# Optimization experiments

Hardware: AMD Instinct MI355X
Metric: run time of the kernel (lower is better)

Reference implementation:

```python
import jax, jax.numpy as jnp
import numpy as np

EPS = 1e-6

def _phi(x):
    # ELU + 1 feature map: strictly positive
    return jax.nn.elu(x) + 1.0

def setup_inputs() -> dict:
    key = jax.random.key(0)
    kq, kk, kv = jax.random.split(key, 3)
    B, T, H, D = 4, 8192, 16, 64
    q = jax.random.normal(kq, (B, T, H, D), dtype=jnp.float32)
    k = jax.random.normal(kk, (B, T, H, D), dtype=jnp.float32)
    v = jax.random.normal(kv, (B, T, H, D), dtype=jnp.float32)
    return {"q": q, "k": k, "v": v}

def _linear_attention(q, k, v):
    # q,k,v: [B,T,H,D] -> out [B,T,H,D]
    phi_q = _phi(q)
    phi_k = _phi(k)
    # time-major for scan: [T,B,H,D]
    pq = jnp.moveaxis(phi_q, 1, 0)
    pk = jnp.moveaxis(phi_k, 1, 0)
    vv = jnp.moveaxis(v, 1, 0)
    B, H, D = pq.shape[1], pq.shape[2], pq.shape[3]
    S0 = jnp.zeros((B, H, D, D), dtype=q.dtype)
    z0 = jnp.zeros((B, H, D), dtype=q.dtype)

    def step(carry, inp):
        S, z = carry
        q_t, k_t, v_t = inp  # each [B,H,D]
        S = S + k_t[..., :, None] * v_t[..., None, :]  # [B,H,D,D]
        z = z + k_t
        num = jnp.einsum('bhd,bhde->bhe', q_t, S)
        den = jnp.einsum('bhd,bhd->bh', q_t, z) + EPS
        return (S, z), num / den[..., None]

    _, out = jax.lax.scan(step, (S0, z0), (pq, pk, vv))
    return jnp.moveaxis(out, 0, 1)  # [B,T,H,D]

def reference(q, k, v):
    return _linear_attention(q, k, v)
```

## Files before the change

kernel.cpp:

```cpp
#include <hip/hip_runtime.h>
#include <hip/hip_bf16.h>


#define EPS_ 1e-6f

constexpr int Bc  = 4;
constexpr int Tc  = 8192;
constexpr int Hc  = 16;
constexpr int Dc  = 64;
constexpr int CH  = 128;
constexpr int NCH = Tc / CH;
constexpr int BHc = Bc * Hc;
constexpr int REC = Dc * Dc + Dc;

typedef short  bf16x8 __attribute__((ext_vector_type(8)));
typedef float  f32x4  __attribute__((ext_vector_type(4)));

__device__ __forceinline__ float phi_f(float x) {
    return x > 0.f ? x + 1.f : __expf(x);
}
__device__ __forceinline__ unsigned short f2b(float x) {
    __hip_bfloat16 b = __float2bfloat16(x);
    return __builtin_bit_cast(unsigned short, b);
}
__device__ __forceinline__ float b2f(unsigned short u) {
    return __uint_as_float(((unsigned)u) << 16);
}

__global__ __launch_bounds__(256) void k_chunksum(const float* __restrict__ kin,
                                                  const float* __restrict__ vin,
                                                  float* __restrict__ ws) {
    const int chunk = blockIdx.x;
    const int bh = chunk >> 6, c = chunk & (NCH - 1);
    const int b  = bh >> 4,    h = bh & 15;
    const int t0 = c * CH;
    const int tid = threadIdx.x;

    __shared__ unsigned short ktr[64][136];
    __shared__ unsigned short vtr[64][136];
    __shared__ float zred[4][64];

    {
        const int srow = tid >> 2;
        const int cb   = (tid & 3) << 4;
        #pragma unroll
        for (int sh = 0; sh < 2; ++sh) {
            const int s = srow + sh * 64;
            const size_t g = ((((size_t)b * Tc) + (t0 + s)) * Hc + h) * Dc + cb;
            const float4* kp = (const float4*)(kin + g);
            const float4* vp = (const float4*)(vin + g);
            #pragma unroll
            for (int i = 0; i < 4; i++) {
                float4 kk = kp[i];
                float4 vv = vp[i];
                ktr[cb + i*4 + 0][s] = f2b(phi_f(kk.x));
                ktr[cb + i*4 + 1][s] = f2b(phi_f(kk.y));
                ktr[cb + i*4 + 2][s] = f2b(phi_f(kk.z));
                ktr[cb + i*4 + 3][s] = f2b(phi_f(kk.w));
                vtr[cb + i*4 + 0][s] = f2b(vv.x);
                vtr[cb + i*4 + 1][s] = f2b(vv.y);
                vtr[cb + i*4 + 2][s] = f2b(vv.z);
                vtr[cb + i*4 + 3][s] = f2b(vv.w);
            }
        }
    }
    __syncthreads();

    {
        const int d = tid & 63, part = tid >> 6;
        float zs = 0.f;
        #pragma unroll
        for (int j = 0; j < 4; j++) {
            bf16x8 kv = *(const bf16x8*)&ktr[d][part * 32 + j * 8];
            #pragma unroll
            for (int u = 0; u < 8; u++) zs += b2f((unsigned short)kv[u]);
        }
        zred[part][d] = zs;
    }

    const int w = tid >> 6, lane = tid & 63;
    const int l15 = lane & 15, quad = lane >> 4;
    f32x4 acc[4];
    #pragma unroll
    for (int nt = 0; nt < 4; nt++) acc[nt] = (f32x4){0.f, 0.f, 0.f, 0.f};
    #pragma unroll
    for (int ks = 0; ks < 4; ks++) {
        bf16x8 a = *(const bf16x8*)&vtr[16 * w + l15][quad * 8 + ks * 32];
        #pragma unroll
        for (int nt = 0; nt < 4; nt++) {
            bf16x8 bb = *(const bf16x8*)&ktr[16 * nt + l15][quad * 8 + ks * 32];
            acc[nt] = __builtin_amdgcn_mfma_f32_16x16x32_bf16(a, bb, acc[nt], 0, 0, 0);
        }
    }
    __syncthreads();

    float* rec = ws + (size_t)chunk * REC;
    #pragma unroll
    for (int nt = 0; nt < 4; nt++)
        #pragma unroll
        for (int r = 0; r < 4; r++) {
            const int e = 16 * w + quad * 4 + r;
            const int d = 16 * nt + l15;
            rec[e * 64 + d] = acc[nt][r];
        }
    if (tid < 64)
        rec[4096 + tid] = zred[0][tid] + zred[1][tid] + zred[2][tid] + zred[3][tid];
}

__global__ __launch_bounds__(256) void k_prefix(float* __restrict__ ws) {
    const int bh = blockIdx.x;
    const int e  = blockIdx.y * 256 + threadIdx.x;
    if (e >= REC) return;
    float* p = ws + (size_t)bh * NCH * REC + e;
    float run = 0.f;
    for (int c = 0; c < NCH; ++c) {
        float x = p[(size_t)c * REC];
        p[(size_t)c * REC] = run;
        run += x;
    }
}

__global__ __launch_bounds__(256) void k_output(const float* __restrict__ qin,
                                                const float* __restrict__ kin,
                                                const float* __restrict__ vin,
                                                const float* __restrict__ ws,
                                                float* __restrict__ outp) {
    const int unit = blockIdx.x;
    const int bh   = unit >> 7;
    const int rem  = unit & (NCH * 2 - 1);
    const int c    = rem >> 1;
    const int half = rem & 1;
    const int b = bh >> 4, h = bh & 15;
    const int t0 = c * CH + half * 64;
    const int tid = threadIdx.x;
    const int w = tid >> 6, lane = tid & 63;
    const int l15 = lane & 15, quad = lane >> 4;

    __shared__ unsigned short qb[64][72];
    __shared__ unsigned short swb[64][72];
    __shared__ unsigned short kb[64][72];
    __shared__ unsigned short vb[64][72];
    __shared__ float zsh[64];
    __shared__ float den[64];

    {
        const int row = tid >> 2, cb = (tid & 3) << 4;
        const float4* qp = (const float4*)(qin + ((((size_t)b * Tc) + (t0 + row)) * Hc + h) * Dc + cb);
        #pragma unroll
        for (int i = 0; i < 4; i++) {
            float4 qq = qp[i];
            unsigned short* dst = &qb[row][cb + i * 4];
            dst[0] = f2b(phi_f(qq.x)); dst[1] = f2b(phi_f(qq.y));
            dst[2] = f2b(phi_f(qq.z)); dst[3] = f2b(phi_f(qq.w));
        }
    }
    {
        const float* rec = ws + (size_t)(bh * NCH + c) * REC;
        #pragma unroll
        for (int i = 0; i < 4; i++) {
            const int idx = tid + i * 256;
            float4 sv = ((const float4*)rec)[idx];
            const int flat = idx * 4, e = flat >> 6, d = flat & 63;
            unsigned short* dst = &swb[e][d];
            dst[0] = f2b(sv.x); dst[1] = f2b(sv.y); dst[2] = f2b(sv.z); dst[3] = f2b(sv.w);
        }
        if (tid < 16) {
            float4 zv = ((const float4*)(rec + 4096))[tid];
            zsh[tid * 4 + 0] = zv.x; zsh[tid * 4 + 1] = zv.y;
            zsh[tid * 4 + 2] = zv.z; zsh[tid * 4 + 3] = zv.w;
        }
    }
    __syncthreads();

    if (tid < 64) {
        float s = 0.f;
        #pragma unroll
        for (int j = 0; j < 8; j++) {
            bf16x8 qv = *(const bf16x8*)&qb[tid][j * 8];
            #pragma unroll
            for (int u = 0; u < 8; u++) s += b2f((unsigned short)qv[u]) * zsh[j * 8 + u];
        }
        den[tid] = s + EPS_;
    }

    f32x4 acc[4];
    #pragma unroll
    for (int nt = 0; nt < 4; nt++) acc[nt] = (f32x4){0.f, 0.f, 0.f, 0.f};
    #pragma unroll
    for (int ks = 0; ks < 2; ks++) {
        bf16x8 a = *(const bf16x8*)&qb[16 * w + l15][quad * 8 + ks * 32];
        #pragma unroll
        for (int nt = 0; nt < 4; nt++) {
            bf16x8 bb = *(const bf16x8*)&swb[16 * nt + l15][quad * 8 + ks * 32];
            acc[nt] = __builtin_amdgcn_mfma_f32_16x16x32_bf16(a, bb, acc[nt], 0, 0, 0);
        }
    }

    for (int st = 0; st <= half; ++st) {
        __syncthreads();
        {
            const int row = tid >> 2, cb = (tid & 3) << 4;
            const int sg = c * CH + st * 64 + row;
            const size_t g = ((((size_t)b * Tc) + sg) * Hc + h) * Dc + cb;
            const float4* kp = (const float4*)(kin + g);
            const float4* vp = (const float4*)(vin + g);
            #pragma unroll
            for (int i = 0; i < 4; i++) {
                float4 kk = kp[i];
                float4 vv = vp[i];
                unsigned short* kd = &kb[row][cb + i * 4];
                kd[0] = f2b(phi_f(kk.x)); kd[1] = f2b(phi_f(kk.y));
                kd[2] = f2b(phi_f(kk.z)); kd[3] = f2b(phi_f(kk.w));
                vb[cb + i * 4 + 0][row] = f2b(vv.x);
                vb[cb + i * 4 + 1][row] = f2b(vv.y);
                vb[cb + i * 4 + 2][row] = f2b(vv.z);
                vb[cb + i * 4 + 3][row] = f2b(vv.w);
            }
        }
        __syncthreads();

        f32x4 wt[4];
        #pragma unroll
        for (int nt = 0; nt < 4; nt++) wt[nt] = (f32x4){0.f, 0.f, 0.f, 0.f};
        #pragma unroll
        for (int ks = 0; ks < 2; ks++) {
            bf16x8 a = *(const bf16x8*)&qb[16 * w + l15][quad * 8 + ks * 32];
            #pragma unroll
            for (int nt = 0; nt < 4; nt++) {
                bf16x8 bb = *(const bf16x8*)&kb[16 * nt + l15][quad * 8 + ks * 32];
                wt[nt] = __builtin_amdgcn_mfma_f32_16x16x32_bf16(a, bb, wt[nt], 0, 0, 0);
            }
        }

        const int tbase = half * 64 + 16 * w + quad * 4;
        float rsum[4] = {0.f, 0.f, 0.f, 0.f};
        #pragma unroll
        for (int nt = 0; nt < 4; nt++) {
            const int sch = st * 64 + 16 * nt + l15;
            #pragma unroll
            for (int r = 0; r < 4; r++) {
                float val = (sch > tbase + r) ? 0.f : wt[nt][r];
                unsigned short wb16 = f2b(val);
                swb[16 * w + quad * 4 + r][16 * nt + l15] = wb16;
                rsum[r] += b2f(wb16);
            }
        }
        #pragma unroll
        for (int r = 0; r < 4; r++) {
            float rs = rsum[r];
            rs += __shfl_xor(rs, 8, 16);
            rs += __shfl_xor(rs, 4, 16);
            rs += __shfl_xor(rs, 2, 16);
            rs += __shfl_xor(rs, 1, 16);
            if (l15 == 0) den[16 * w + quad * 4 + r] += rs;
        }
        __syncthreads();

        #pragma unroll
        for (int ks = 0; ks < 2; ks++) {
            bf16x8 a = *(const bf16x8*)&swb[16 * w + l15][quad * 8 + ks * 32];
            #pragma unroll
            for (int nt = 0; nt < 4; nt++) {
                bf16x8 bb = *(const bf16x8*)&vb[16 * nt + l15][quad * 8 + ks * 32];
                acc[nt] = __builtin_amdgcn_mfma_f32_16x16x32_bf16(a, bb, acc[nt], 0, 0, 0);
            }
        }
    }
    __syncthreads();

    #pragma unroll
    for (int r = 0; r < 4; r++) {
        const int t = 16 * w + quad * 4 + r;
        const float inv = 1.0f / den[t];
        const size_t gbase = ((((size_t)b * Tc) + (t0 + t)) * Hc + h) * Dc;
        #pragma unroll
        for (int nt = 0; nt < 4; nt++) {
            outp[gbase + 16 * nt + l15] = acc[nt][r] * inv;
        }
    }
}

extern "C" void kernel_launch(void* const* d_in, const int* in_sizes, int n_in,
                              void* d_out, int out_size, void* d_ws, size_t ws_size,
                              hipStream_t stream) {
    const float* q = (const float*)d_in[0];
    const float* k = (const float*)d_in[1];
    const float* v = (const float*)d_in[2];
    float* out = (float*)d_out;
    float* ws  = (float*)d_ws;

    k_chunksum<<<BHc * NCH, 256, 0, stream>>>(k, v, ws);
    dim3 g2(BHc, (REC + 255) / 256);
    k_prefix<<<g2, 256, 0, stream>>>(ws);
    k_output<<<BHc * NCH * 2, 256, 0, stream>>>(q, k, v, ws, out);
}
```

Baseline: 541.9 us.

## Process full 128-row chunk per output block and vectorize transposed LDS stores

The output kernel now handles a whole 128-token chunk per 512-thread block instead of two 64-token halves. This removes the duplicate reload and phi of the first half's keys/values and of the chunk-state S. It computes the intra-chunk QK^T once, with upper waves doing extra tiles, and reuses the qb/kb buffers for the masked weights. The chunksum and V transposes now store 4 bf16 values at once via ushort4 instead of scalar strided stores. The prefix loop gets an unroll hint. The cost is larger LDS per block and uneven work across waves.

Measured after the change: 516.5 us. 1.05x faster.

```diff
diff --git a/kernel.cpp b/kernel.cpp
--- a/kernel.cpp
+++ b/kernel.cpp
@@ -41,26 +41,26 @@
     __shared__ float zred[4][64];
 
     {
-        const int srow = tid >> 2;
-        const int cb   = (tid & 3) << 4;
+        const int c0 = (tid & 15) << 2;
+        const int rl = ((tid >> 4) & 15) << 2;
         #pragma unroll
         for (int sh = 0; sh < 2; ++sh) {
-            const int s = srow + sh * 64;
-            const size_t g = ((((size_t)b * Tc) + (t0 + s)) * Hc + h) * Dc + cb;
-            const float4* kp = (const float4*)(kin + g);
-            const float4* vp = (const float4*)(vin + g);
-            #pragma unroll
-            for (int i = 0; i < 4; i++) {
-                float4 kk = kp[i];
-                float4 vv = vp[i];
-                ktr[cb + i*4 + 0][s] = f2b(phi_f(kk.x));
-                ktr[cb + i*4 + 1][s] = f2b(phi_f(kk.y));
-                ktr[cb + i*4 + 2][s] = f2b(phi_f(kk.z));
-                ktr[cb + i*4 + 3][s] = f2b(phi_f(kk.w));
-                vtr[cb + i*4 + 0][s] = f2b(vv.x);
-                vtr[cb + i*4 + 1][s] = f2b(vv.y);
-                vtr[cb + i*4 + 2][s] = f2b(vv.z);
-                vtr[cb + i*4 + 3][s] = f2b(vv.w);
+            const int r0 = rl + sh * 64;
+            unsigned short hk[4][4], hv[4][4];
+            #pragma unroll
+            for (int jj = 0; jj < 4; ++jj) {
+                const size_t g = ((((size_t)b * Tc) + (t0 + r0 + jj)) * Hc + h) * Dc + c0;
+                const float4 kk = *(const float4*)(kin + g);
+                const float4 vv = *(const float4*)(vin + g);
+                hk[jj][0] = f2b(phi_f(kk.x)); hk[jj][1] = f2b(phi_f(kk.y));
+                hk[jj][2] = f2b(phi_f(kk.z)); hk[jj][3] = f2b(phi_f(kk.w));
+                hv[jj][0] = f2b(vv.x); hv[jj][1] = f2b(vv.y);
+                hv[jj][2] = f2b(vv.z); hv[jj][3] = f2b(vv.w);
+            }
+            #pragma unroll
+            for (int j = 0; j < 4; ++j) {
+                *(ushort4*)&ktr[c0 + j][r0] = make_ushort4(hk[0][j], hk[1][j], hk[2][j], hk[3][j]);
+                *(ushort4*)&vtr[c0 + j][r0] = make_ushort4(hv[0][j], hv[1][j], hv[2][j], hv[3][j]);
             }
         }
     }
@@ -113,6 +113,7 @@
     if (e >= REC) return;
     float* p = ws + (size_t)bh * NCH * REC + e;
     float run = 0.f;
+    #pragma unroll 4
     for (int c = 0; c < NCH; ++c) {
         float x = p[(size_t)c * REC];
         p[(size_t)c * REC] = run;
@@ -120,49 +121,64 @@
     }
 }
 
-__global__ __launch_bounds__(256) void k_output(const float* __restrict__ qin,
-                                                const float* __restrict__ kin,
-                                                const float* __restrict__ vin,
-                                                const float* __restrict__ ws,
-                                                float* __restrict__ outp) {
-    const int unit = blockIdx.x;
-    const int bh   = unit >> 7;
-    const int rem  = unit & (NCH * 2 - 1);
-    const int c    = rem >> 1;
-    const int half = rem & 1;
+__global__ __launch_bounds__(512, 4) void k_output(const float* __restrict__ qin,
+                                                   const float* __restrict__ kin,
+                                                   const float* __restrict__ vin,
+                                                   const float* __restrict__ ws,
+                                                   float* __restrict__ outp) {
+    const int chunk = blockIdx.x;
+    const int bh = chunk >> 6, c = chunk & (NCH - 1);
     const int b = bh >> 4, h = bh & 15;
-    const int t0 = c * CH + half * 64;
+    const int t0 = c * CH;
     const int tid = threadIdx.x;
     const int w = tid >> 6, lane = tid & 63;
     const int l15 = lane & 15, quad = lane >> 4;
 
-    __shared__ unsigned short qb[64][72];
-    __shared__ unsigned short swb[64][72];
-    __shared__ unsigned short kb[64][72];
-    __shared__ unsigned short vb[64][72];
+    __shared__ unsigned short qb[128][72];
+    __shared__ unsigned short kb[128][72];
+    __shared__ unsigned short sb[64][72];
+    __shared__ unsigned short vb[64][136];
     __shared__ float zsh[64];
-    __shared__ float den[64];
+    __shared__ float den[128];
 
     {
         const int row = tid >> 2, cb = (tid & 3) << 4;
-        const float4* qp = (const float4*)(qin + ((((size_t)b * Tc) + (t0 + row)) * Hc + h) * Dc + cb);
+        const size_t g = ((((size_t)b * Tc) + (t0 + row)) * Hc + h) * Dc + cb;
+        const float4* qp = (const float4*)(qin + g);
+        const float4* kp = (const float4*)(kin + g);
         #pragma unroll
         for (int i = 0; i < 4; i++) {
             float4 qq = qp[i];
-            unsigned short* dst = &qb[row][cb + i * 4];
-            dst[0] = f2b(phi_f(qq.x)); dst[1] = f2b(phi_f(qq.y));
-            dst[2] = f2b(phi_f(qq.z)); dst[3] = f2b(phi_f(qq.w));
-        }
-    }
-    {
-        const float* rec = ws + (size_t)(bh * NCH + c) * REC;
-        #pragma unroll
-        for (int i = 0; i < 4; i++) {
-            const int idx = tid + i * 256;
+            float4 kk = kp[i];
+            *(ushort4*)&qb[row][cb + 4 * i] =
+                make_ushort4(f2b(phi_f(qq.x)), f2b(phi_f(qq.y)), f2b(phi_f(qq.z)), f2b(phi_f(qq.w)));
+            *(ushort4*)&kb[row][cb + 4 * i] =
+                make_ushort4(f2b(phi_f(kk.x)), f2b(phi_f(kk.y)), f2b(phi_f(kk.z)), f2b(phi_f(kk.w)));
+        }
+    }
+    {
+        const int c0 = (tid & 15) << 2;
+        const int r0 = (tid >> 4) << 2;
+        unsigned short hv[4][4];
+        #pragma unroll
+        for (int jj = 0; jj < 4; ++jj) {
+            const size_t g = ((((size_t)b * Tc) + (t0 + r0 + jj)) * Hc + h) * Dc + c0;
+            const float4 vv = *(const float4*)(vin + g);
+            hv[jj][0] = f2b(vv.x); hv[jj][1] = f2b(vv.y);
+            hv[jj][2] = f2b(vv.z); hv[jj][3] = f2b(vv.w);
+        }
+        #pragma unroll
+        for (int j = 0; j < 4; ++j)
+            *(ushort4*)&vb[c0 + j][r0] = make_ushort4(hv[0][j], hv[1][j], hv[2][j], hv[3][j]);
+    }
+    {
+        const float* rec = ws + (size_t)chunk * REC;
+        #pragma unroll
+        for (int i = 0; i < 2; i++) {
+            const int idx = tid + i * 512;
             float4 sv = ((const float4*)rec)[idx];
             const int flat = idx * 4, e = flat >> 6, d = flat & 63;
-            unsigned short* dst = &swb[e][d];
-            dst[0] = f2b(sv.x); dst[1] = f2b(sv.y); dst[2] = f2b(sv.z); dst[3] = f2b(sv.w);
+            *(ushort4*)&sb[e][d] = make_ushort4(f2b(sv.x), f2b(sv.y), f2b(sv.z), f2b(sv.w));
         }
         if (tid < 16) {
             float4 zv = ((const float4*)(rec + 4096))[tid];
@@ -172,7 +188,7 @@
     }
     __syncthreads();
 
-    if (tid < 64) {
+    if (tid < 128) {
         float s = 0.f;
         #pragma unroll
         for (int j = 0; j < 8; j++) {
@@ -191,58 +207,57 @@
         bf16x8 a = *(const bf16x8*)&qb[16 * w + l15][quad * 8 + ks * 32];
         #pragma unroll
         for (int nt = 0; nt < 4; nt++) {
-            bf16x8 bb = *(const bf16x8*)&swb[16 * nt + l15][quad * 8 + ks * 32];
+            bf16x8 bb = *(const bf16x8*)&sb[16 * nt + l15][quad * 8 + ks * 32];
             acc[nt] = __builtin_amdgcn_mfma_f32_16x16x32_bf16(a, bb, acc[nt], 0, 0, 0);
         }
     }
 
-    for (int st = 0; st <= half; ++st) {
-        __syncthreads();
-        {
-            const int row = tid >> 2, cb = (tid & 3) << 4;
-            const int sg = c * CH + st * 64 + row;
-            const size_t g = ((((size_t)b * Tc) + sg) * Hc + h) * Dc + cb;
-            const float4* kp = (const float4*)(kin + g);
-            const float4* vp = (const float4*)(vin + g);
-            #pragma unroll
-            for (int i = 0; i < 4; i++) {
-                float4 kk = kp[i];
-                float4 vv = vp[i];
-                unsigned short* kd = &kb[row][cb + i * 4];
-                kd[0] = f2b(phi_f(kk.x)); kd[1] = f2b(phi_f(kk.y));
-                kd[2] = f2b(phi_f(kk.z)); kd[3] = f2b(phi_f(kk.w));
-                vb[cb + i * 4 + 0][row] = f2b(vv.x);
-                vb[cb + i * 4 + 1][row] = f2b(vv.y);
-                vb[cb + i * 4 + 2][row] = f2b(vv.z);
-                vb[cb + i * 4 + 3][row] = f2b(vv.w);
-            }
-        }
-        __syncthreads();
-
-        f32x4 wt[4];
-        #pragma unroll
-        for (int nt = 0; nt < 4; nt++) wt[nt] = (f32x4){0.f, 0.f, 0.f, 0.f};
-        #pragma unroll
-        for (int ks = 0; ks < 2; ks++) {
-            bf16x8 a = *(const bf16x8*)&qb[16 * w + l15][quad * 8 + ks * 32];
-            #pragma unroll
-            for (int nt = 0; nt < 4; nt++) {
+    f32x4 wt[8];
+    #pragma unroll
+    for (int nt = 0; nt < 8; nt++) wt[nt] = (f32x4){0.f, 0.f, 0.f, 0.f};
+    #pragma unroll
+    for (int ks = 0; ks < 2; ks++) {
+        bf16x8 a = *(const bf16x8*)&qb[16 * w + l15][quad * 8 + ks * 32];
+        #pragma unroll
+        for (int nt = 0; nt < 4; nt++) {
+            bf16x8 bb = *(const bf16x8*)&kb[16 * nt + l15][quad * 8 + ks * 32];
+            wt[nt] = __builtin_amdgcn_mfma_f32_16x16x32_bf16(a, bb, wt[nt], 0, 0, 0);
+        }
+        if (w >= 4) {
+            #pragma unroll
+            for (int nt = 4; nt < 8; nt++) {
                 bf16x8 bb = *(const bf16x8*)&kb[16 * nt + l15][quad * 8 + ks * 32];
                 wt[nt] = __builtin_amdgcn_mfma_f32_16x16x32_bf16(a, bb, wt[nt], 0, 0, 0);
             }
         }
-
-        const int tbase = half * 64 + 16 * w + quad * 4;
+    }
+    __syncthreads();
+
+    {
+        const int tbase = 16 * w + quad * 4;
         float rsum[4] = {0.f, 0.f, 0.f, 0.f};
         #pragma unroll
         for (int nt = 0; nt < 4; nt++) {
-            const int sch = st * 64 + 16 * nt + l15;
+            const int s = 16 * nt + l15;
             #pragma unroll
             for (int r = 0; r < 4; r++) {
-                float val = (sch > tbase + r) ? 0.f : wt[nt][r];
+                float val = (s > tbase + r) ? 0.f : wt[nt][r];
                 unsigned short wb16 = f2b(val);
-                swb[16 * w + quad * 4 + r][16 * nt + l15] = wb16;
+                kb[tbase + r][s] = wb16;
                 rsum[r] += b2f(wb16);
+            }
+        }
+        if (w >= 4) {
+            #pragma unroll
+            for (int nt = 4; nt < 8; nt++) {
+                const int s = 16 * nt + l15;
+                #pragma unroll
+                for (int r = 0; r < 4; r++) {
+                    float val = (s > tbase + r) ? 0.f : wt[nt][r];
+                    unsigned short wb16 = f2b(val);
+                    qb[tbase + r][s - 64] = wb16;
+                    rsum[r] += b2f(wb16);
+                }
             }
         }
         #pragma unroll
@@ -252,13 +267,24 @@
             rs += __shfl_xor(rs, 4, 16);
             rs += __shfl_xor(rs, 2, 16);
             rs += __shfl_xor(rs, 1, 16);
-            if (l15 == 0) den[16 * w + quad * 4 + r] += rs;
-        }
-        __syncthreads();
-
-        #pragma unroll
-        for (int ks = 0; ks < 2; ks++) {
-            bf16x8 a = *(const bf16x8*)&swb[16 * w + l15][quad * 8 + ks * 32];
+            if (l15 == 0) den[tbase + r] += rs;
+        }
+    }
+    __syncthreads();
+
+    #pragma unroll
+    for (int ks = 0; ks < 2; ks++) {
+        bf16x8 a = *(const bf16x8*)&kb[16 * w + l15][quad * 8 + ks * 32];
+        #pragma unroll
+        for (int nt = 0; nt < 4; nt++) {
+            bf16x8 bb = *(const bf16x8*)&vb[16 * nt + l15][quad * 8 + ks * 32];
+            acc[nt] = __builtin_amdgcn_mfma_f32_16x16x32_bf16(a, bb, acc[nt], 0, 0, 0);
+        }
+    }
+    if (w >= 4) {
+        #pragma unroll
+        for (int ks = 2; ks < 4; ks++) {
+            bf16x8 a = *(const bf16x8*)&qb[16 * w + l15][quad * 8 + (ks - 2) * 32];
             #pragma unroll
             for (int nt = 0; nt < 4; nt++) {
                 bf16x8 bb = *(const bf16x8*)&vb[16 * nt + l15][quad * 8 + ks * 32];
@@ -266,7 +292,6 @@
             }
         }
     }
-    __syncthreads();
 
     #pragma unroll
     for (int r = 0; r < 4; r++) {
@@ -292,5 +317,5 @@
     k_chunksum<<<BHc * NCH, 256, 0, stream>>>(k, v, ws);
     dim3 g2(BHc, (REC + 255) / 256);
     k_prefix<<<g2, 256, 0, stream>>>(ws);
-    k_output<<<BHc * NCH * 2, 256, 0, stream>>>(q, k, v, ws, out);
-}
+    k_output<<<BHc * NCH, 512, 0, stream>>>(q, k, v, ws, out);
+}
```
